# Kernel optimization log

Measured on AMD Instinct MI355X. Metric: run time of the kernel, lower is better.

The kernel has to match this reference:

```python
import jax, jax.numpy as jnp
import numpy as np

N, C, D = 16384, 1000, 1024

def setup_inputs() -> dict:
    key = jax.random.key(0)
    k1, k2 = jax.random.split(key)
    embedding = jax.random.normal(k1, (N, D), dtype=jnp.float32)
    # nn.Parameter init is zeros in the module, but zeros give degenerate (all-equal)
    # distances; use random centers as a trained-parameter stand-in.
    centers = jax.random.normal(k2, (C, D), dtype=jnp.float32)
    return {"embedding": embedding, "centers": centers}

def reference(embedding, centers):
    # pytorch_ood.utils.pairwise_distances: squared Euclidean via norm + matmul trick
    x_norm = jnp.sum(embedding * embedding, axis=1, keepdims=True)      # [N, 1]
    y_norm = jnp.sum(centers * centers, axis=1)[None, :]                # [1, C]
    dist = x_norm + y_norm - 2.0 * jnp.matmul(embedding, centers.T)     # [N, C]
    return jnp.maximum(dist, 0.0)
```

## Files before the change

### kernel.cpp

```cpp
#include <hip/hip_runtime.h>
#include <hip/hip_bf16.h>
#include <stdint.h>

#define N_ROWS 16384
#define C_ROWS 1000
#define C_PAD  1024
#define D_DIM  1024

#define BM 128
#define BN 128
#define BK 32
#define KSTEPS (D_DIM / BK)
#define TILE_ELEMS (BM * BK)

typedef __attribute__((ext_vector_type(8))) short    bf16x8;
typedef __attribute__((ext_vector_type(4))) float    f32x4;
typedef __attribute__((ext_vector_type(4))) uint32_t u32x4;

__device__ __forceinline__ uint32_t pk2bf(float lo, float hi) {
    union { float f; uint32_t u; } a, b;
    a.f = lo; b.f = hi;
    uint32_t l = (a.u + 0x8000u) >> 16;
    uint32_t h = (b.u + 0x8000u) >> 16;
    return l | (h << 16);
}

__device__ __forceinline__ void gl_lds16(const uint16_t* g, uint16_t* l) {
    __builtin_amdgcn_global_load_lds(
        (const __attribute__((address_space(1))) void*)g,
        (__attribute__((address_space(3))) void*)l,
        16, 0, 0);
}

__global__ void convert_norm_tiled(const float* __restrict__ x,
                                   uint16_t* __restrict__ xt,
                                   float* __restrict__ norms,
                                   int rows, int pad_rows) {
    int wid  = (blockIdx.x * blockDim.x + threadIdx.x) >> 6;
    int lane = threadIdx.x & 63;
    if (wid >= pad_rows) return;
    const int tile = wid >> 7;
    const int row  = wid & 127;
    uint16_t* tbase = xt + (size_t)tile * KSTEPS * TILE_ELEMS;
    const int kslot = lane & 3;
    const int cellb = (kslot * 128 + row) * 8;
    if (wid < rows) {
        const f32x4* rp = (const f32x4*)(x + (size_t)wid * D_DIM);
        float s = 0.f;
#pragma unroll
        for (int i = 0; i < 2; ++i) {
            f32x4 v0 = rp[i * 128 + lane * 2];
            f32x4 v1 = rp[i * 128 + lane * 2 + 1];
            s += v0[0]*v0[0] + v0[1]*v0[1] + v0[2]*v0[2] + v0[3]*v0[3]
               + v1[0]*v1[0] + v1[1]*v1[1] + v1[2]*v1[2] + v1[3]*v1[3];
            u32x4 p;
            p[0] = pk2bf(v0[0], v0[1]); p[1] = pk2bf(v0[2], v0[3]);
            p[2] = pk2bf(v1[0], v1[1]); p[3] = pk2bf(v1[2], v1[3]);
            const int t = i * 16 + (lane >> 2);
            *(u32x4*)(tbase + (size_t)t * TILE_ELEMS + cellb) = p;
        }
#pragma unroll
        for (int off = 32; off > 0; off >>= 1) s += __shfl_down(s, off, 64);
        if (lane == 0) norms[wid] = s;
    } else {
        u32x4 z = {0, 0, 0, 0};
#pragma unroll
        for (int i = 0; i < 2; ++i) {
            const int t = i * 16 + (lane >> 2);
            *(u32x4*)(tbase + (size_t)t * TILE_ELEMS + cellb) = z;
        }
        if (lane == 0) norms[wid] = 0.f;
    }
}

__global__ __launch_bounds__(256, 4)
void dist_gemm2(const uint16_t* __restrict__ At,
                const uint16_t* __restrict__ Bt,
                const float* __restrict__ xn,
                const float* __restrict__ yn,
                float* __restrict__ out) {
    __shared__ uint16_t As[2][TILE_ELEMS];
    __shared__ uint16_t Bs[2][TILE_ELEMS];

    const int tid  = threadIdx.x;
    const int lane = tid & 63;
    const int wid  = tid >> 6;
    const int wm   = wid >> 1;
    const int wn   = wid & 1;

    const int rowTile = blockIdx.x;
    const int colTile = blockIdx.y;

    const uint16_t* Abase = At + (size_t)rowTile * KSTEPS * TILE_ELEMS;
    const uint16_t* Bbase = Bt + (size_t)colTile * KSTEPS * TILE_ELEMS;

    const int off0 = tid * 8;
    const int off1 = 2048 + tid * 8;

    const int fA = ((lane >> 4) * 128 + wm * 64 + (lane & 15)) * 8;
    const int fB = ((lane >> 4) * 128 + wn * 64 + (lane & 15)) * 8;

    f32x4 acc[4][4];
#pragma unroll
    for (int m = 0; m < 4; ++m)
#pragma unroll
        for (int n = 0; n < 4; ++n) acc[m][n] = (f32x4)(0.f);

#define STAGE(buf, t)                                               \
    do {                                                            \
        const uint16_t* ga = Abase + (size_t)(t) * TILE_ELEMS;      \
        const uint16_t* gb = Bbase + (size_t)(t) * TILE_ELEMS;      \
        gl_lds16(ga + off0, &As[buf][off0]);                        \
        gl_lds16(ga + off1, &As[buf][off1]);                        \
        gl_lds16(gb + off0, &Bs[buf][off0]);                        \
        gl_lds16(gb + off1, &Bs[buf][off1]);                        \
    } while (0)

    STAGE(0, 0);
    __syncthreads();

    int cur = 0;
    for (int t = 0; t < KSTEPS; ++t) {
        if (t + 1 < KSTEPS) STAGE(cur ^ 1, t + 1);
        bf16x8 ar[4], br[4];
#pragma unroll
        for (int m = 0; m < 4; ++m) ar[m] = *(const bf16x8*)&As[cur][fA + m * 16 * 8];
#pragma unroll
        for (int n = 0; n < 4; ++n) br[n] = *(const bf16x8*)&Bs[cur][fB + n * 16 * 8];
#pragma unroll
        for (int m = 0; m < 4; ++m)
#pragma unroll
            for (int n = 0; n < 4; ++n)
                acc[m][n] = __builtin_amdgcn_mfma_f32_16x16x32_bf16(
                    ar[m], br[n], acc[m][n], 0, 0, 0);
        __syncthreads();
        cur ^= 1;
    }
#undef STAGE

    float* Cs = (float*)&As[0][0];
    const int mrow = (lane >> 4) * 4;
    const int ccol = wn * 64 + (lane & 15);
    const int srow = tid >> 4;
    const int scol = (tid & 15) * 4;

#pragma unroll
    for (int p = 0; p < 8; ++p) {
        __syncthreads();
        if (wm == (p >> 2)) {
            const int m = p & 3;
#pragma unroll
            for (int n = 0; n < 4; ++n)
#pragma unroll
                for (int r = 0; r < 4; ++r)
                    Cs[(mrow + r) * 132 + ccol + n * 16] = acc[m][n][r];
        }
        __syncthreads();
        const int grow = rowTile * BM + p * 16 + srow;
        const float xr = xn[grow];
        float* orow = out + (size_t)grow * C_ROWS;
#pragma unroll
        for (int s = 0; s < 2; ++s) {
            const int c  = scol + s * 64;
            const int gc = colTile * BN + c;
            f32x4 d = *(f32x4*)&Cs[srow * 132 + c];
            f32x4 y4 = *(const f32x4*)&yn[gc];
            f32x4 v;
#pragma unroll
            for (int j = 0; j < 4; ++j)
                v[j] = fmaxf(xr + y4[j] - 2.0f * d[j], 0.f);
            if (gc + 3 < C_ROWS) {
                *(f32x4*)&orow[gc] = v;
            } else {
#pragma unroll
                for (int j = 0; j < 4; ++j)
                    if (gc + j < C_ROWS) orow[gc + j] = v[j];
            }
        }
    }
}

__global__ void row_norms_kernel(const float* __restrict__ x,
                                 float* __restrict__ out,
                                 int rows, int pad_rows) {
    int gid  = blockIdx.x * blockDim.x + threadIdx.x;
    int wid  = gid >> 6;
    int lane = threadIdx.x & 63;
    if (wid >= pad_rows) return;
    float s = 0.f;
    if (wid < rows) {
        const f32x4* rp = (const f32x4*)(x + (size_t)wid * D_DIM);
#pragma unroll
        for (int r = 0; r < D_DIM / 256; ++r) {
            f32x4 v = rp[r * 64 + lane];
            s += v[0]*v[0] + v[1]*v[1] + v[2]*v[2] + v[3]*v[3];
        }
    }
#pragma unroll
    for (int off = 32; off > 0; off >>= 1) s += __shfl_down(s, off, 64);
    if (lane == 0) out[wid] = s;
}

__global__ __launch_bounds__(256, 2)
void dist_gemm_kernel(const float* __restrict__ E,
                      const float* __restrict__ Cc,
                      const float* __restrict__ xn,
                      const float* __restrict__ yn,
                      float* __restrict__ out) {
    __shared__ uint16_t As[4 * 128 * 8];
    __shared__ uint16_t Bs[4 * 128 * 8];
    const int tid  = threadIdx.x;
    const int lane = tid & 63;
    const int wid  = tid >> 6;
    const int wm   = wid >> 1;
    const int wn   = wid & 1;
    const int rowTile = blockIdx.y;
    const int colTile = blockIdx.x;
    const int srow = tid & 127;
    const int sp   = tid >> 7;
    const int ga = rowTile * 128 + srow;
    const int gb = colTile * 128 + srow;
    const float* Arow = E  + (size_t)ga * D_DIM + sp * 16;
    const float* Brow = Cc + (size_t)gb * D_DIM + sp * 16;
    const bool bvalid = (gb < C_ROWS);
    f32x4 acc[4][4];
#pragma unroll
    for (int m = 0; m < 4; ++m)
#pragma unroll
        for (int n = 0; n < 4; ++n) acc[m][n] = (f32x4)(0.f);
    const int fragA_base = (((lane >> 4) * 128) + wm * 64 + (lane & 15)) * 8;
    const int fragB_base = (((lane >> 4) * 128) + wn * 64 + (lane & 15)) * 8;
    const int stA0 = ((sp * 2) * 128 + srow) * 8;
    const int stA1 = ((sp * 2 + 1) * 128 + srow) * 8;
    for (int k0 = 0; k0 < D_DIM; k0 += 32) {
        f32x4 a0 = *(const f32x4*)(Arow + k0);
        f32x4 a1 = *(const f32x4*)(Arow + k0 + 4);
        f32x4 a2 = *(const f32x4*)(Arow + k0 + 8);
        f32x4 a3 = *(const f32x4*)(Arow + k0 + 12);
        f32x4 b0 = (f32x4)(0.f), b1 = (f32x4)(0.f),
              b2 = (f32x4)(0.f), b3 = (f32x4)(0.f);
        if (bvalid) {
            b0 = *(const f32x4*)(Brow + k0);
            b1 = *(const f32x4*)(Brow + k0 + 4);
            b2 = *(const f32x4*)(Brow + k0 + 8);
            b3 = *(const f32x4*)(Brow + k0 + 12);
        }
        u32x4 pa01, pa23, pb01, pb23;
        pa01[0] = pk2bf(a0[0], a0[1]); pa01[1] = pk2bf(a0[2], a0[3]);
        pa01[2] = pk2bf(a1[0], a1[1]); pa01[3] = pk2bf(a1[2], a1[3]);
        pa23[0] = pk2bf(a2[0], a2[1]); pa23[1] = pk2bf(a2[2], a2[3]);
        pa23[2] = pk2bf(a3[0], a3[1]); pa23[3] = pk2bf(a3[2], a3[3]);
        pb01[0] = pk2bf(b0[0], b0[1]); pb01[1] = pk2bf(b0[2], b0[3]);
        pb01[2] = pk2bf(b1[0], b1[1]); pb01[3] = pk2bf(b1[2], b1[3]);
        pb23[0] = pk2bf(b2[0], b2[1]); pb23[1] = pk2bf(b2[2], b2[3]);
        pb23[2] = pk2bf(b3[0], b3[1]); pb23[3] = pk2bf(b3[2], b3[3]);
        __syncthreads();
        *(u32x4*)&As[stA0] = pa01;
        *(u32x4*)&As[stA1] = pa23;
        *(u32x4*)&Bs[stA0] = pb01;
        *(u32x4*)&Bs[stA1] = pb23;
        __syncthreads();
        bf16x8 ar[4], br[4];
#pragma unroll
        for (int m = 0; m < 4; ++m) ar[m] = *(const bf16x8*)&As[fragA_base + m * 16 * 8];
#pragma unroll
        for (int n = 0; n < 4; ++n) br[n] = *(const bf16x8*)&Bs[fragB_base + n * 16 * 8];
#pragma unroll
        for (int m = 0; m < 4; ++m)
#pragma unroll
            for (int n = 0; n < 4; ++n)
                acc[m][n] = __builtin_amdgcn_mfma_f32_16x16x32_bf16(
                    ar[m], br[n], acc[m][n], 0, 0, 0);
    }
    const int orow0 = rowTile * 128 + wm * 64 + ((lane >> 4) * 4);
    const int ocol0 = colTile * 128 + wn * 64 + (lane & 15);
#pragma unroll
    for (int n = 0; n < 4; ++n) {
        int gc = ocol0 + n * 16;
        if (gc >= C_ROWS) continue;
        float ynv = yn[gc];
#pragma unroll
        for (int m = 0; m < 4; ++m) {
            int gr = orow0 + m * 16;
#pragma unroll
            for (int r = 0; r < 4; ++r) {
                float v = xn[gr + r] + ynv - 2.0f * acc[m][n][r];
                out[(size_t)(gr + r) * C_ROWS + gc] = fmaxf(v, 0.f);
            }
        }
    }
}

extern "C" void kernel_launch(void* const* d_in, const int* in_sizes, int n_in,
                              void* d_out, int out_size, void* d_ws, size_t ws_size,
                              hipStream_t stream) {
    const float* E  = (const float*)d_in[0];
    const float* Cc = (const float*)d_in[1];
    float* out = (float*)d_out;

    uint16_t* Et = (uint16_t*)d_ws;
    uint16_t* Ct = Et + (size_t)N_ROWS * D_DIM;
    float*    xn = (float*)(Ct + (size_t)C_PAD * D_DIM);
    float*    yn = xn + N_ROWS;
    size_t need = (size_t)((char*)(yn + C_PAD) - (char*)d_ws);

    if (ws_size >= need) {
        convert_norm_tiled<<<N_ROWS / 4, 256, 0, stream>>>(E,  Et, xn, N_ROWS, N_ROWS);
        convert_norm_tiled<<<C_PAD  / 4, 256, 0, stream>>>(Cc, Ct, yn, C_ROWS, C_PAD);
        dim3 grid(N_ROWS / BM, C_PAD / BN);
        dist_gemm2<<<grid, 256, 0, stream>>>(Et, Ct, xn, yn, out);
    } else {
        float* fxn = (float*)d_ws;
        float* fyn = fxn + N_ROWS;
        row_norms_kernel<<<N_ROWS / 4, 256, 0, stream>>>(E,  fxn, N_ROWS, N_ROWS);
        row_norms_kernel<<<C_PAD  / 4, 256, 0, stream>>>(Cc, fyn, C_ROWS, C_PAD);
        dim3 grid(C_PAD / 128, N_ROWS / 128);
        dist_gemm_kernel<<<grid, 256, 0, stream>>>(E, Cc, fxn, fyn, out);
    }
}
```

Before: 66.90 us.

## Fuse embedding bf16 conversion and row norms into the GEMM main loop

Drops the separate pass that converts the embedding matrix to tiled bf16 and computes its row norms. The GEMM now loads fp32 embedding rows directly into registers, accumulates the squared norm, packs to bf16 and writes to LDS during the MFMA phase, and keeps only the small centers conversion kernel. This removes a full read and write of the converted embedding and one launch. In exchange each column-tile block re-reads the fp32 embedding (8 times in total, at twice the bytes of bf16) and uses more registers, which may lower occupancy.

```diff
diff --git a/kernel.cpp b/kernel.cpp
--- a/kernel.cpp
+++ b/kernel.cpp
@@ -32,20 +32,19 @@
         16, 0, 0);
 }
 
-__global__ void convert_norm_tiled(const float* __restrict__ x,
-                                   uint16_t* __restrict__ xt,
-                                   float* __restrict__ norms,
-                                   int rows, int pad_rows) {
+__global__ void convert_norm_c(const float* __restrict__ Cc,
+                               uint16_t* __restrict__ Ct,
+                               float* __restrict__ yn) {
     int wid  = (blockIdx.x * blockDim.x + threadIdx.x) >> 6;
     int lane = threadIdx.x & 63;
-    if (wid >= pad_rows) return;
+    if (wid >= C_PAD) return;
     const int tile = wid >> 7;
     const int row  = wid & 127;
-    uint16_t* tbase = xt + (size_t)tile * KSTEPS * TILE_ELEMS;
+    uint16_t* tbase = Ct + (size_t)tile * KSTEPS * TILE_ELEMS;
     const int kslot = lane & 3;
     const int cellb = (kslot * 128 + row) * 8;
-    if (wid < rows) {
-        const f32x4* rp = (const f32x4*)(x + (size_t)wid * D_DIM);
+    if (wid < C_ROWS) {
+        const f32x4* rp = (const f32x4*)(Cc + (size_t)wid * D_DIM);
         float s = 0.f;
 #pragma unroll
         for (int i = 0; i < 2; ++i) {
@@ -61,7 +60,7 @@
         }
 #pragma unroll
         for (int off = 32; off > 0; off >>= 1) s += __shfl_down(s, off, 64);
-        if (lane == 0) norms[wid] = s;
+        if (lane == 0) yn[wid] = s;
     } else {
         u32x4 z = {0, 0, 0, 0};
 #pragma unroll
@@ -69,18 +68,18 @@
             const int t = i * 16 + (lane >> 2);
             *(u32x4*)(tbase + (size_t)t * TILE_ELEMS + cellb) = z;
         }
-        if (lane == 0) norms[wid] = 0.f;
+        if (lane == 0) yn[wid] = 0.f;
     }
 }
 
 __global__ __launch_bounds__(256, 4)
-void dist_gemm2(const uint16_t* __restrict__ At,
+void dist_gemm7(const float* __restrict__ E,
                 const uint16_t* __restrict__ Bt,
-                const float* __restrict__ xn,
                 const float* __restrict__ yn,
                 float* __restrict__ out) {
     __shared__ uint16_t As[2][TILE_ELEMS];
     __shared__ uint16_t Bs[2][TILE_ELEMS];
+    __shared__ float xrow[128];
 
     const int tid  = threadIdx.x;
     const int lane = tid & 63;
@@ -91,9 +90,13 @@
     const int rowTile = blockIdx.x;
     const int colTile = blockIdx.y;
 
-    const uint16_t* Abase = At + (size_t)rowTile * KSTEPS * TILE_ELEMS;
+    const int arow = tid >> 1;
+    const float* Ap = E + (size_t)(rowTile * BM + arow) * D_DIM + (tid & 1) * 16;
+    const int wk = (tid & 1) * 2;
+    const int wd0 = (wk * 128 + arow) * 8;
+    const int wd1 = ((wk + 1) * 128 + arow) * 8;
+
     const uint16_t* Bbase = Bt + (size_t)colTile * KSTEPS * TILE_ELEMS;
-
     const int off0 = tid * 8;
     const int off1 = 2048 + tid * 8;
 
@@ -106,22 +109,47 @@
 #pragma unroll
         for (int n = 0; n < 4; ++n) acc[m][n] = (f32x4)(0.f);
 
-#define STAGE(buf, t)                                               \
-    do {                                                            \
-        const uint16_t* ga = Abase + (size_t)(t) * TILE_ELEMS;      \
-        const uint16_t* gb = Bbase + (size_t)(t) * TILE_ELEMS;      \
-        gl_lds16(ga + off0, &As[buf][off0]);                        \
-        gl_lds16(ga + off1, &As[buf][off1]);                        \
-        gl_lds16(gb + off0, &Bs[buf][off0]);                        \
-        gl_lds16(gb + off1, &Bs[buf][off1]);                        \
+    float s = 0.f;
+    f32x4 ra0, ra1, ra2, ra3;
+
+#define LOADA(t)                                            \
+    do {                                                    \
+        const float* p = Ap + (t) * BK;                     \
+        ra0 = *(const f32x4*)(p);                           \
+        ra1 = *(const f32x4*)(p + 4);                       \
+        ra2 = *(const f32x4*)(p + 8);                       \
+        ra3 = *(const f32x4*)(p + 12);                      \
     } while (0)
 
-    STAGE(0, 0);
+#define CVTWR(buf)                                                          \
+    do {                                                                    \
+        s += ra0[0]*ra0[0] + ra0[1]*ra0[1] + ra0[2]*ra0[2] + ra0[3]*ra0[3]  \
+           + ra1[0]*ra1[0] + ra1[1]*ra1[1] + ra1[2]*ra1[2] + ra1[3]*ra1[3]  \
+           + ra2[0]*ra2[0] + ra2[1]*ra2[1] + ra2[2]*ra2[2] + ra2[3]*ra2[3]  \
+           + ra3[0]*ra3[0] + ra3[1]*ra3[1] + ra3[2]*ra3[2] + ra3[3]*ra3[3]; \
+        u32x4 w0, w1;                                                       \
+        w0[0] = pk2bf(ra0[0], ra0[1]); w0[1] = pk2bf(ra0[2], ra0[3]);       \
+        w0[2] = pk2bf(ra1[0], ra1[1]); w0[3] = pk2bf(ra1[2], ra1[3]);       \
+        w1[0] = pk2bf(ra2[0], ra2[1]); w1[1] = pk2bf(ra2[2], ra2[3]);       \
+        w1[2] = pk2bf(ra3[0], ra3[1]); w1[3] = pk2bf(ra3[2], ra3[3]);       \
+        *(u32x4*)&As[buf][wd0] = w0;                                        \
+        *(u32x4*)&As[buf][wd1] = w1;                                        \
+    } while (0)
+
+#define STAGEB(buf, t)                                                      \
+    do {                                                                    \
+        const uint16_t* gb = Bbase + (size_t)(t) * TILE_ELEMS;              \
+        gl_lds16(gb + off0, &Bs[buf][off0]);                                \
+        gl_lds16(gb + off1, &Bs[buf][off1]);                                \
+    } while (0)
+
+    LOADA(0); STAGEB(0, 0);
+    CVTWR(0);
     __syncthreads();
 
     int cur = 0;
     for (int t = 0; t < KSTEPS; ++t) {
-        if (t + 1 < KSTEPS) STAGE(cur ^ 1, t + 1);
+        if (t + 1 < KSTEPS) { LOADA(t + 1); STAGEB(cur ^ 1, t + 1); }
         bf16x8 ar[4], br[4];
 #pragma unroll
         for (int m = 0; m < 4; ++m) ar[m] = *(const bf16x8*)&As[cur][fA + m * 16 * 8];
@@ -133,10 +161,17 @@
             for (int n = 0; n < 4; ++n)
                 acc[m][n] = __builtin_amdgcn_mfma_f32_16x16x32_bf16(
                     ar[m], br[n], acc[m][n], 0, 0, 0);
+        if (t + 1 < KSTEPS) CVTWR(cur ^ 1);
         __syncthreads();
         cur ^= 1;
     }
-#undef STAGE
+#undef LOADA
+#undef CVTWR
+#undef STAGEB
+
+    s += __shfl_xor(s, 1, 64);
+    if ((tid & 1) == 0) xrow[arow] = s;
+    __syncthreads();
 
     float* Cs = (float*)&As[0][0];
     const int mrow = (lane >> 4) * 4;
@@ -156,12 +191,13 @@
                     Cs[(mrow + r) * 132 + ccol + n * 16] = acc[m][n][r];
         }
         __syncthreads();
-        const int grow = rowTile * BM + p * 16 + srow;
-        const float xr = xn[grow];
+        const int lrow = p * 16 + srow;
+        const int grow = rowTile * BM + lrow;
+        const float xr = xrow[lrow];
         float* orow = out + (size_t)grow * C_ROWS;
 #pragma unroll
-        for (int s = 0; s < 2; ++s) {
-            const int c  = scol + s * 64;
+        for (int ss = 0; ss < 2; ++ss) {
+            const int c  = scol + ss * 64;
             const int gc = colTile * BN + c;
             f32x4 d = *(f32x4*)&Cs[srow * 132 + c];
             f32x4 y4 = *(const f32x4*)&yn[gc];
@@ -298,17 +334,14 @@
     const float* Cc = (const float*)d_in[1];
     float* out = (float*)d_out;
 
-    uint16_t* Et = (uint16_t*)d_ws;
-    uint16_t* Ct = Et + (size_t)N_ROWS * D_DIM;
-    float*    xn = (float*)(Ct + (size_t)C_PAD * D_DIM);
-    float*    yn = xn + N_ROWS;
+    uint16_t* Ct = (uint16_t*)d_ws;
+    float*    yn = (float*)(Ct + (size_t)C_PAD * D_DIM);
     size_t need = (size_t)((char*)(yn + C_PAD) - (char*)d_ws);
 
     if (ws_size >= need) {
-        convert_norm_tiled<<<N_ROWS / 4, 256, 0, stream>>>(E,  Et, xn, N_ROWS, N_ROWS);
-        convert_norm_tiled<<<C_PAD  / 4, 256, 0, stream>>>(Cc, Ct, yn, C_ROWS, C_PAD);
+        convert_norm_c<<<C_PAD / 4, 256, 0, stream>>>(Cc, Ct, yn);
         dim3 grid(N_ROWS / BM, C_PAD / BN);
-        dist_gemm2<<<grid, 256, 0, stream>>>(Et, Ct, xn, yn, out);
+        dist_gemm7<<<grid, 256, 0, stream>>>(E, Ct, yn, out);
     } else {
         float* fxn = (float*)d_ws;
         float* fyn = fxn + N_ROWS;
```

Result: slower. 74.24 us (+11.0%).
